# Kernel optimization log

Measured on AMD Instinct MI355X. Metric: run time of the kernel, lower is better.

The kernel has to match this reference:

```python
import jax, jax.numpy as jnp
import numpy as np

TAU = 2.0      # LIF membrane time constant (spikingjelly LIFNode tau=2.0)
V_TH = 1.0     # default spikingjelly threshold
ALPHA = 2.0    # ATan surrogate default alpha

@jax.custom_vjp
def atan_spike(x):
    # Heaviside forward, ATan surrogate backward (spikingjelly surrogate.ATan)
    return (x >= 0.0).astype(x.dtype)

def _spike_fwd(x):
    return atan_spike(x), x

def _spike_bwd(x, g):
    sg = (ALPHA / 2.0) / (1.0 + (jnp.pi / 2.0 * ALPHA * x) ** 2)
    return (g * sg,)

atan_spike.defvjp(_spike_fwd, _spike_bwd)


def setup_inputs() -> dict:
    key = jax.random.key(0)
    ks = jax.random.split(key, 4)
    B, L, C, H, NL, K = 64, 96, 32, 256, 2, 3
    inputs = jax.random.normal(ks[0], (B, L, C), jnp.float32)
    w_enc = jax.random.normal(ks[1], (H, 1, K), jnp.float32) * (1.0 / np.sqrt(K))
    b_enc = jnp.zeros((H,), jnp.float32)
    w_rnn = jax.random.normal(ks[2], (NL, H, H), jnp.float32) * (1.0 / np.sqrt(H))
    b_rnn = jnp.zeros((NL, H), jnp.float32)
    return {"inputs": inputs, "w_enc": w_enc, "b_enc": b_enc,
            "w_rnn": w_rnn, "b_rnn": b_rnn}


def reference(inputs, w_enc, b_enc, w_rnn, b_rnn):
    B, L, C = inputs.shape
    H = w_enc.shape[0]
    NL = w_rnn.shape[0]
    # --- 'conv' spike encoder: per-channel temporal conv -> [B*C, H, L] ---
    x = inputs.transpose(0, 2, 1).reshape(B * C, 1, L)
    h = jax.lax.conv_general_dilated(x, w_enc, (1,), 'SAME',
                                     dimension_numbers=('NCH', 'OIH', 'NCH'))
    h = h + b_enc[None, :, None]
    h = h.transpose(2, 0, 1)  # [L, B*C, H] time-major for scan

    def step(v, x_t):
        s = x_t
        new_v = []
        for l in range(NL):  # fixed small layer loop
            cur = s @ w_rnn[l].T + b_rnn[l]            # Linear
            vl = v[l] + (cur - v[l]) / TAU             # leaky integrate
            s = atan_spike(vl - V_TH)                  # fire (surrogate grad)
            vl = vl * (1.0 - jax.lax.stop_gradient(s)) # hard reset, detach_reset
            new_v.append(vl)
        return tuple(new_v), (s, new_v[-1])

    v0 = tuple(jnp.zeros((B * C, H), inputs.dtype) for _ in range(NL))
    _, (spks, mems) = jax.lax.scan(step, v0, h)
    # spks: [L, B*C, H] -> [B, C*H, L]
    spks = spks.reshape(L, B, C * H).transpose(1, 2, 0)
    return spks.transpose(0, 2, 1), spks[:, :, -1]
```

## Files before the change

### kernel.cpp

```cpp
#include <hip/hip_runtime.h>
#include <hip/hip_bf16.h>
#include <stdint.h>


using short8  = __attribute__((ext_vector_type(8))) short;
using floatx4 = __attribute__((ext_vector_type(4))) float;

__device__ __forceinline__ unsigned short f2bf(float f) {
    unsigned int u = __float_as_uint(f);
    unsigned int r = u + 0x7fffu + ((u >> 16) & 1u);
    return (unsigned short)(r >> 16);
}
__device__ __forceinline__ float bf2f(unsigned short h) {
    return __uint_as_float(((unsigned int)h) << 16);
}

__device__ __forceinline__ uint4 expand8(unsigned int byte) {
    unsigned int lo = ((byte & 0xFu) * 0x00204081u) & 0x01010101u;
    unsigned int hi = (((byte >> 4) & 0xFu) * 0x00204081u) & 0x01010101u;
    uint4 d;
    d.x = __builtin_amdgcn_perm(0u, lo, 0x04010400u) * 0x3F80u;
    d.y = __builtin_amdgcn_perm(0u, lo, 0x04030402u) * 0x3F80u;
    d.z = __builtin_amdgcn_perm(0u, hi, 0x04010400u) * 0x3F80u;
    d.w = __builtin_amdgcn_perm(0u, hi, 0x04030402u) * 0x3F80u;
    return d;
}

__global__ void prep_kernel(const float* __restrict__ w_enc,
                            const float* __restrict__ b_enc,
                            const float* __restrict__ w_rnn,
                            const float* __restrict__ b_rnn,
                            double* __restrict__ Wd,
                            double* __restrict__ C0d,
                            unsigned short* __restrict__ Bw)
{
    const int o = blockIdx.x;
    const int lane = threadIdx.x;
    const float4 w0v = *(const float4*)(w_rnn + (size_t)o * 256 + lane * 4);
    double a0 = 0.0, a1 = 0.0, a2 = 0.0, ab = 0.0;
#pragma unroll
    for (int e = 0; e < 4; ++e) {
        const int i = lane * 4 + e;
        const double wv = (double)(((const float*)&w0v)[e]);
        a0 += wv * (double)w_enc[i * 3 + 0];
        a1 += wv * (double)w_enc[i * 3 + 1];
        a2 += wv * (double)w_enc[i * 3 + 2];
        ab += wv * (double)b_enc[i];
    }
    for (int off = 32; off > 0; off >>= 1) {
        a0 += __shfl_down(a0, off, 64);
        a1 += __shfl_down(a1, off, 64);
        a2 += __shfl_down(a2, off, 64);
        ab += __shfl_down(ab, off, 64);
    }
    if (lane == 0) {
        Wd[o * 3 + 0] = a0;
        Wd[o * 3 + 1] = a1;
        Wd[o * 3 + 2] = a2;
        C0d[o] = ab + (double)b_rnn[o];
    }
    const float4 w1v = *(const float4*)(w_rnn + 65536 + (size_t)o * 256 + lane * 4);
    ushort4 hi, mi, lo;
#pragma unroll
    for (int e = 0; e < 4; ++e) {
        float f = ((const float*)&w1v)[e];
        unsigned short h = f2bf(f);
        float r1 = f - bf2f(h);
        unsigned short mm = f2bf(r1);
        float r2 = r1 - bf2f(mm);
        unsigned short ll = f2bf(r2);
        ((unsigned short*)&hi)[e] = h;
        ((unsigned short*)&mi)[e] = mm;
        ((unsigned short*)&lo)[e] = ll;
    }
    *(ushort4*)(Bw + (size_t)o * 768 + lane * 4)       = hi;
    *(ushort4*)(Bw + (size_t)o * 768 + 256 + lane * 4) = mi;
    *(ushort4*)(Bw + (size_t)o * 768 + 512 + lane * 4) = lo;
}

__global__ void enc_kernel(const float* __restrict__ inputs,
                           const double* __restrict__ Wd,
                           const double* __restrict__ C0d,
                           unsigned long long* __restrict__ s0b)
{
    const int n = blockIdx.x;
    const int tidx = threadIdx.x;
    const int b = n >> 5, c = n & 31;
    __shared__ float xr[98];
    if (tidx < 96)       xr[tidx + 1] = inputs[((size_t)b * 96 + tidx) * 32 + c];
    else if (tidx == 96) xr[0]  = 0.0f;
    else if (tidx == 97) xr[97] = 0.0f;
    __syncthreads();
    const double W0 = Wd[tidx * 3], W1 = Wd[tidx * 3 + 1], W2 = Wd[tidx * 3 + 2];
    const double c0 = C0d[tidx];
    const int wid = tidx >> 6, lane = tidx & 63;
    float v = 0.0f;
    for (int t = 0; t < 96; ++t) {
        float cur = (float)((double)xr[t] * W0 + (double)xr[t + 1] * W1 +
                            (double)xr[t + 2] * W2 + c0);
        float vv = v + (cur - v) * 0.5f;
        int sp = (vv - 1.0f) >= 0.0f;
        v = sp ? 0.0f : vv;
        unsigned long long bal = __ballot(sp);
        if (lane == 0) s0b[((size_t)t * 2048 + n) * 4 + wid] = bal;
    }
}

__global__ __launch_bounds__(256, 2) void rnn_kernel(
    const unsigned char* __restrict__ s0b,
    const unsigned short* __restrict__ Bw,
    const float* __restrict__ b_rnn,
    float* __restrict__ out0,
    float* __restrict__ out1)
{
    const int tid  = threadIdx.x;
    const int wid  = tid >> 6, lane = tid & 63;
    const int m    = lane & 15, g = lane >> 4;
    const int g8   = g * 8;
    const int rt   = blockIdx.x >> 2;
    const int nw   = rt * 16;
    const int o0   = (blockIdx.x & 3) * 64 + wid * 16;

    short8 bfrag[24];
#pragma unroll
    for (int ks = 0; ks < 24; ++ks)
        bfrag[ks] = *(const short8*)(Bw + (size_t)(o0 + m) * 768 + ks * 32 + g8);
    const float bias = b_rnn[256 + o0 + m];

    float* pr[4];
    int    row_r[4];
#pragma unroll
    for (int r = 0; r < 4; ++r) {
        const int row = nw + g * 4 + r;
        row_r[r] = row;
        pr[r] = out0 + ((size_t)(row >> 5) * 96) * 8192 + (size_t)(row & 31) * 256
                     + o0 + m;
    }

    const unsigned char* mbase = s0b + ((size_t)(nw + m)) * 32;
    uint4 ma0 = *(const uint4*)(mbase);
    uint4 mb0 = *(const uint4*)(mbase + 16);
    uint4 ma1 = *(const uint4*)(mbase + 65536);
    uint4 mb1 = *(const uint4*)(mbase + 65536 + 16);

    floatx4 v = {0.f, 0.f, 0.f, 0.f};

#pragma unroll 2
    for (int t = 0; t < 96; ++t) {
        uint4 pa = ma1, pb = mb1;
        if (t < 94) {
            const unsigned char* q = mbase + (size_t)(t + 2) * 65536;
            ma1 = *(const uint4*)q;
            mb1 = *(const uint4*)(q + 16);
        }

        unsigned int w32[8] = {ma0.x, ma0.y, ma0.z, ma0.w,
                               mb0.x, mb0.y, mb0.z, mb0.w};
        short8 af[8];
#pragma unroll
        for (int f = 0; f < 8; ++f) {
            uint4 e = expand8((w32[f] >> g8) & 0xFFu);
            af[f] = *(short8*)&e;
        }

        floatx4 acc = {0.f, 0.f, 0.f, 0.f};
#pragma unroll
        for (int ks = 0; ks < 24; ++ks)
            acc = __builtin_amdgcn_mfma_f32_16x16x32_bf16(af[ks & 7], bfrag[ks], acc, 0, 0, 0);

#pragma unroll
        for (int r = 0; r < 4; ++r) {
            float cur = acc[r] + bias;
            float vv = v[r];
            vv = vv + (cur - vv) * 0.5f;
            float s = ((vv - 1.0f) >= 0.0f) ? 1.0f : 0.0f;
            v[r] = vv * (1.0f - s);
            pr[r][(size_t)t * 8192] = s;
            if (t == 95)
                out1[(size_t)row_r[r] * 256 + o0 + m] = s;
        }
        ma0 = pa; mb0 = pb;
    }
}

extern "C" void kernel_launch(void* const* d_in, const int* in_sizes, int n_in,
                              void* d_out, int out_size, void* d_ws, size_t ws_size,
                              hipStream_t stream) {
    const float* inputs = (const float*)d_in[0];
    const float* w_enc  = (const float*)d_in[1];
    const float* b_enc  = (const float*)d_in[2];
    const float* w_rnn  = (const float*)d_in[3];
    const float* b_rnn  = (const float*)d_in[4];

    float* out0 = (float*)d_out;
    float* out1 = out0 + (size_t)64 * 96 * 8192;

    char* ws = (char*)d_ws;
    double*         Wd  = (double*)(ws);
    double*         C0d = (double*)(ws + 6144);
    unsigned short* Bw  = (unsigned short*)(ws + 8192);
    char*           s0b = ws + 401408;

    prep_kernel<<<256, 64, 0, stream>>>(w_enc, b_enc, w_rnn, b_rnn, Wd, C0d, Bw);
    enc_kernel<<<2048, 256, 0, stream>>>(inputs, Wd, C0d, (unsigned long long*)s0b);
    rnn_kernel<<<512, 256, 0, stream>>>((const unsigned char*)s0b, Bw, b_rnn, out0, out1);
}
```

Before: 295.4 us.

## Replace bf16x3 split MFMA with int8 four-limb fixed-point MFMA for layer-2 matmul

Layer-2 weights are now quantized to 27-bit fixed point and split into four signed int8 limbs. The recurrent matmul then uses i32_16x16x64_i8 MFMAs on 0/1 spike bytes in place of 24 bf16 MFMAs with a three-way split. The limb results are recombined exactly in integer and double arithmetic. The spike bitmask layout and the wave-to-tile job mapping also change so each lane reads 8 bytes. The goal is fewer MFMA instructions and cheaper spike expansion per step, at the cost of a fixed-point rounding of the weights that could flip spikes near threshold.

```diff
diff --git a/kernel.cpp b/kernel.cpp
--- a/kernel.cpp
+++ b/kernel.cpp
@@ -3,28 +3,8 @@
 #include <stdint.h>
 
 
-using short8  = __attribute__((ext_vector_type(8))) short;
 using floatx4 = __attribute__((ext_vector_type(4))) float;
-
-__device__ __forceinline__ unsigned short f2bf(float f) {
-    unsigned int u = __float_as_uint(f);
-    unsigned int r = u + 0x7fffu + ((u >> 16) & 1u);
-    return (unsigned short)(r >> 16);
-}
-__device__ __forceinline__ float bf2f(unsigned short h) {
-    return __uint_as_float(((unsigned int)h) << 16);
-}
-
-__device__ __forceinline__ uint4 expand8(unsigned int byte) {
-    unsigned int lo = ((byte & 0xFu) * 0x00204081u) & 0x01010101u;
-    unsigned int hi = (((byte >> 4) & 0xFu) * 0x00204081u) & 0x01010101u;
-    uint4 d;
-    d.x = __builtin_amdgcn_perm(0u, lo, 0x04010400u) * 0x3F80u;
-    d.y = __builtin_amdgcn_perm(0u, lo, 0x04030402u) * 0x3F80u;
-    d.z = __builtin_amdgcn_perm(0u, hi, 0x04010400u) * 0x3F80u;
-    d.w = __builtin_amdgcn_perm(0u, hi, 0x04030402u) * 0x3F80u;
-    return d;
-}
+using intx4   = __attribute__((ext_vector_type(4))) int;
 
 __global__ void prep_kernel(const float* __restrict__ w_enc,
                             const float* __restrict__ b_enc,
@@ -32,7 +12,7 @@
                             const float* __restrict__ b_rnn,
                             double* __restrict__ Wd,
                             double* __restrict__ C0d,
-                            unsigned short* __restrict__ Bw)
+                            signed char* __restrict__ Bw8)
 {
     const int o = blockIdx.x;
     const int lane = threadIdx.x;
@@ -60,28 +40,29 @@
         C0d[o] = ab + (double)b_rnn[o];
     }
     const float4 w1v = *(const float4*)(w_rnn + 65536 + (size_t)o * 256 + lane * 4);
-    ushort4 hi, mi, lo;
+    unsigned int pack[4] = {0u, 0u, 0u, 0u};
 #pragma unroll
     for (int e = 0; e < 4; ++e) {
         float f = ((const float*)&w1v)[e];
-        unsigned short h = f2bf(f);
-        float r1 = f - bf2f(h);
-        unsigned short mm = f2bf(r1);
-        float r2 = r1 - bf2f(mm);
-        unsigned short ll = f2bf(r2);
-        ((unsigned short*)&hi)[e] = h;
-        ((unsigned short*)&mi)[e] = mm;
-        ((unsigned short*)&lo)[e] = ll;
-    }
-    *(ushort4*)(Bw + (size_t)o * 768 + lane * 4)       = hi;
-    *(ushort4*)(Bw + (size_t)o * 768 + 256 + lane * 4) = mi;
-    *(ushort4*)(Bw + (size_t)o * 768 + 512 + lane * 4) = lo;
+        int q = __double2int_rn((double)f * 134217728.0);
+        int d3 = ((q + 64) & 127) - 64;  q = (q - d3) >> 7;
+        int d2 = ((q + 64) & 127) - 64;  q = (q - d2) >> 7;
+        int d1 = ((q + 64) & 127) - 64;  q = (q - d1) >> 7;
+        int d0 = q;
+        pack[0] |= ((unsigned int)(d0 & 0xFF)) << (8 * e);
+        pack[1] |= ((unsigned int)(d1 & 0xFF)) << (8 * e);
+        pack[2] |= ((unsigned int)(d2 & 0xFF)) << (8 * e);
+        pack[3] |= ((unsigned int)(d3 & 0xFF)) << (8 * e);
+    }
+#pragma unroll
+    for (int l = 0; l < 4; ++l)
+        *(unsigned int*)(Bw8 + ((size_t)o * 4 + l) * 256 + lane * 4) = pack[l];
 }
 
 __global__ void enc_kernel(const float* __restrict__ inputs,
                            const double* __restrict__ Wd,
                            const double* __restrict__ C0d,
-                           unsigned long long* __restrict__ s0b)
+                           unsigned char* __restrict__ s0b)
 {
     const int n = blockIdx.x;
     const int tidx = threadIdx.x;
@@ -102,13 +83,17 @@
         int sp = (vv - 1.0f) >= 0.0f;
         v = sp ? 0.0f : vv;
         unsigned long long bal = __ballot(sp);
-        if (lane == 0) s0b[((size_t)t * 2048 + n) * 4 + wid] = bal;
+        if ((lane & 15) == 0) {
+            const int j = lane >> 4;
+            *(unsigned short*)(s0b + ((size_t)t * 2048 + n) * 32 + 8 * j + 2 * wid)
+                = (unsigned short)(bal >> (16 * j));
+        }
     }
 }
 
 __global__ __launch_bounds__(256, 2) void rnn_kernel(
     const unsigned char* __restrict__ s0b,
-    const unsigned short* __restrict__ Bw,
+    const signed char* __restrict__ Bw8,
     const float* __restrict__ b_rnn,
     float* __restrict__ out0,
     float* __restrict__ out1)
@@ -116,15 +101,18 @@
     const int tid  = threadIdx.x;
     const int wid  = tid >> 6, lane = tid & 63;
     const int m    = lane & 15, g = lane >> 4;
-    const int g8   = g * 8;
-    const int rt   = blockIdx.x >> 2;
+    const int job  = blockIdx.x * 4 + wid;
+    const int rt   = job >> 4;
     const int nw   = rt * 16;
-    const int o0   = (blockIdx.x & 3) * 64 + wid * 16;
-
-    short8 bfrag[24];
-#pragma unroll
-    for (int ks = 0; ks < 24; ++ks)
-        bfrag[ks] = *(const short8*)(Bw + (size_t)(o0 + m) * 768 + ks * 32 + g8);
+    const int o0   = (job & 15) * 16;
+
+    intx4 bfrag[4][4];
+#pragma unroll
+    for (int l = 0; l < 4; ++l)
+#pragma unroll
+        for (int c = 0; c < 4; ++c)
+            bfrag[l][c] = *(const intx4*)(Bw8 + ((size_t)(o0 + m) * 4 + l) * 256
+                                               + c * 64 + g * 16);
     const float bias = b_rnn[256 + o0 + m];
 
     float* pr[4];
@@ -137,40 +125,46 @@
                      + o0 + m;
     }
 
-    const unsigned char* mbase = s0b + ((size_t)(nw + m)) * 32;
-    uint4 ma0 = *(const uint4*)(mbase);
-    uint4 mb0 = *(const uint4*)(mbase + 16);
-    uint4 ma1 = *(const uint4*)(mbase + 65536);
-    uint4 mb1 = *(const uint4*)(mbase + 65536 + 16);
+    const unsigned char* mp = s0b + ((size_t)(nw + m)) * 32 + 8 * g;
+    uint2 m0 = *(const uint2*)(mp);
+    uint2 m1 = *(const uint2*)(mp + 65536);
 
     floatx4 v = {0.f, 0.f, 0.f, 0.f};
 
-#pragma unroll 2
     for (int t = 0; t < 96; ++t) {
-        uint4 pa = ma1, pb = mb1;
-        if (t < 94) {
-            const unsigned char* q = mbase + (size_t)(t + 2) * 65536;
-            ma1 = *(const uint4*)q;
-            mb1 = *(const uint4*)(q + 16);
-        }
-
-        unsigned int w32[8] = {ma0.x, ma0.y, ma0.z, ma0.w,
-                               mb0.x, mb0.y, mb0.z, mb0.w};
-        short8 af[8];
-#pragma unroll
-        for (int f = 0; f < 8; ++f) {
-            uint4 e = expand8((w32[f] >> g8) & 0xFFu);
-            af[f] = *(short8*)&e;
-        }
-
-        floatx4 acc = {0.f, 0.f, 0.f, 0.f};
-#pragma unroll
-        for (int ks = 0; ks < 24; ++ks)
-            acc = __builtin_amdgcn_mfma_f32_16x16x32_bf16(af[ks & 7], bfrag[ks], acc, 0, 0, 0);
+        uint2 pa = m1;
+        if (t < 94)
+            m1 = *(const uint2*)(mp + (size_t)(t + 2) * 65536);
+
+        unsigned int hw[4] = { m0.x & 0xFFFFu, m0.x >> 16,
+                               m0.y & 0xFFFFu, m0.y >> 16 };
+        intx4 af[4];
+#pragma unroll
+        for (int c = 0; c < 4; ++c) {
+            unsigned int h = hw[c];
+            intx4 a;
+            a.x = (int)((( h        & 0xFu) * 0x00204081u) & 0x01010101u);
+            a.y = (int)((((h >> 4)  & 0xFu) * 0x00204081u) & 0x01010101u);
+            a.z = (int)((((h >> 8)  & 0xFu) * 0x00204081u) & 0x01010101u);
+            a.w = (int)((((h >> 12) & 0xFu) * 0x00204081u) & 0x01010101u);
+            af[c] = a;
+        }
+
+        intx4 acc0 = {0,0,0,0}, acc1 = {0,0,0,0}, acc2 = {0,0,0,0}, acc3 = {0,0,0,0};
+#pragma unroll
+        for (int c = 0; c < 4; ++c) {
+            acc0 = __builtin_amdgcn_mfma_i32_16x16x64_i8(af[c], bfrag[0][c], acc0, 0, 0, 0);
+            acc1 = __builtin_amdgcn_mfma_i32_16x16x64_i8(af[c], bfrag[1][c], acc1, 0, 0, 0);
+            acc2 = __builtin_amdgcn_mfma_i32_16x16x64_i8(af[c], bfrag[2][c], acc2, 0, 0, 0);
+            acc3 = __builtin_amdgcn_mfma_i32_16x16x64_i8(af[c], bfrag[3][c], acc3, 0, 0, 0);
+        }
 
 #pragma unroll
         for (int r = 0; r < 4; ++r) {
-            float cur = acc[r] + bias;
+            int a01 = acc0[r] * 128 + acc1[r];
+            int a23 = acc2[r] * 128 + acc3[r];
+            double dd = (double)a01 * 16384.0 + (double)a23;
+            float cur = (float)(dd * 7.450580596923828125e-9) + bias;
             float vv = v[r];
             vv = vv + (cur - vv) * 0.5f;
             float s = ((vv - 1.0f) >= 0.0f) ? 1.0f : 0.0f;
@@ -179,7 +173,7 @@
             if (t == 95)
                 out1[(size_t)row_r[r] * 256 + o0 + m] = s;
         }
-        ma0 = pa; mb0 = pb;
+        m0 = pa;
     }
 }
 
@@ -196,12 +190,12 @@
     float* out1 = out0 + (size_t)64 * 96 * 8192;
 
     char* ws = (char*)d_ws;
-    double*         Wd  = (double*)(ws);
-    double*         C0d = (double*)(ws + 6144);
-    unsigned short* Bw  = (unsigned short*)(ws + 8192);
-    char*           s0b = ws + 401408;
-
-    prep_kernel<<<256, 64, 0, stream>>>(w_enc, b_enc, w_rnn, b_rnn, Wd, C0d, Bw);
-    enc_kernel<<<2048, 256, 0, stream>>>(inputs, Wd, C0d, (unsigned long long*)s0b);
-    rnn_kernel<<<512, 256, 0, stream>>>((const unsigned char*)s0b, Bw, b_rnn, out0, out1);
-}
+    double*      Wd  = (double*)(ws);
+    double*      C0d = (double*)(ws + 6144);
+    signed char* Bw8 = (signed char*)(ws + 8192);
+    unsigned char* s0b = (unsigned char*)(ws + 270336);
+
+    prep_kernel<<<256, 64, 0, stream>>>(w_enc, b_enc, w_rnn, b_rnn, Wd, C0d, Bw8);
+    enc_kernel<<<2048, 256, 0, stream>>>(inputs, Wd, C0d, s0b);
+    rnn_kernel<<<512, 256, 0, stream>>>(s0b, Bw8, b_rnn, out0, out1);
+}
```

Measured after the change: 262.2 us. 1.13x faster.
